# Optimization experiments

Measured on AMD Instinct MI355X. Metric: run time of the kernel, lower is better.

## Reference

```python
import jax, jax.numpy as jnp
import numpy as np

EMBED_DIM = 1024
NUM_HEADS = 16
HEAD_DIM = EMBED_DIM // NUM_HEADS


def setup_inputs() -> dict:
    key = jax.random.key(0)
    ks = jax.random.split(key, 9)
    s = 1.0 / np.sqrt(EMBED_DIM)
    x = jax.random.normal(ks[0], (2, 2048, EMBED_DIM), dtype=jnp.float32)
    Wq = jax.random.uniform(ks[1], (EMBED_DIM, EMBED_DIM), jnp.float32, -s, s)
    bq = jax.random.uniform(ks[2], (EMBED_DIM,), jnp.float32, -s, s)
    Wk = jax.random.uniform(ks[3], (EMBED_DIM, EMBED_DIM), jnp.float32, -s, s)
    bk = jax.random.uniform(ks[4], (EMBED_DIM,), jnp.float32, -s, s)
    Wv = jax.random.uniform(ks[5], (EMBED_DIM, EMBED_DIM), jnp.float32, -s, s)
    bv = jax.random.uniform(ks[6], (EMBED_DIM,), jnp.float32, -s, s)
    Wo = jax.random.uniform(ks[7], (EMBED_DIM, EMBED_DIM), jnp.float32, -s, s)
    bo = jax.random.uniform(ks[8], (EMBED_DIM,), jnp.float32, -s, s)
    return {"x": x, "Wq": Wq, "bq": bq, "Wk": Wk, "bk": bk,
            "Wv": Wv, "bv": bv, "Wo": Wo, "bo": bo}


def reference(x, Wq, bq, Wk, bk, Wv, bv, Wo, bo):
    B, N, C = x.shape
    H, D = NUM_HEADS, HEAD_DIM
    # nn.Linear: y = x @ W.T + b; here W stored as [in, out] so y = x @ W + b
    def split_heads(y):
        return y.reshape(B, N, H, D).transpose(0, 2, 1, 3)  # [B,H,N,D]
    q = split_heads(x @ Wq + bq)
    k = split_heads(x @ Wk + bk)
    v = split_heads(x @ Wv + bv)
    scores = jnp.einsum('bhnd,bhmd->bhnm', q, k) / jnp.sqrt(jnp.float32(D)).astype(x.dtype)
    attn = jax.nn.softmax(scores, axis=-1)
    ctx = jnp.einsum('bhnm,bhmd->bhnd', attn, v)
    ctx = ctx.transpose(0, 2, 1, 3).reshape(B, N, C)
    return ctx @ Wo + bo
```

## Files before the change

### kernel.cpp

```cpp
#include <hip/hip_runtime.h>
#include <hip/hip_bf16.h>
#include <stdint.h>
#include <stddef.h>

using bf16 = __hip_bfloat16;
using bf16x8 = __attribute__((ext_vector_type(8))) short;
using f32x4  = __attribute__((ext_vector_type(4))) float;
using f32x16 = __attribute__((ext_vector_type(16))) float;
typedef unsigned int u32x2 __attribute__((ext_vector_type(2)));
typedef unsigned int u32x4 __attribute__((ext_vector_type(4)));

#define MFMA16(a, b, c) __builtin_amdgcn_mfma_f32_16x16x32_bf16((a), (b), (c), 0, 0, 0)
#define MFMA32(a, b, c) __builtin_amdgcn_mfma_f32_32x32x16_bf16((a), (b), (c), 0, 0, 0)

#define GLD16(g, l)                                                            \
  __builtin_amdgcn_global_load_lds(                                            \
      (const __attribute__((address_space(1))) void*)(g),                      \
      (__attribute__((address_space(3))) void*)(l), 16, 0, 0)

__device__ __forceinline__ float exp2_fast(float x) {
#if __has_builtin(__builtin_amdgcn_exp2f)
  return __builtin_amdgcn_exp2f(x);
#else
  return __expf(x * 0.69314718056f);
#endif
}

__device__ __forceinline__ float fmax3(float a, float b, float c) {
  return fmaxf(fmaxf(a, b), c);
}

__device__ __forceinline__ unsigned int cvtpk_bf16(float lo, float hi) {
  unsigned int r;
  asm("v_cvt_pk_bf16_f32 %0, %1, %2" : "=v"(r) : "v"(lo), "v"(hi));
  return r;
}

__device__ __forceinline__ void permswap(unsigned int& a, unsigned int& b, int hi) {
#if __has_builtin(__builtin_amdgcn_permlane32_swap)
  u32x2 r = __builtin_amdgcn_permlane32_swap(a, b, false, false);
  a = r.x;
  b = r.y;
#else
  unsigned int sa = __shfl_xor((unsigned int)a, 32, 64);
  unsigned int sb = __shfl_xor((unsigned int)b, 32, 64);
  unsigned int an = hi ? sb : a;
  unsigned int bn = hi ? b : sa;
  a = an; b = bn;
#endif
}


__global__ void convert_x(const float* __restrict__ x, bf16* __restrict__ out) {
  const int i = blockIdx.x * 256 + threadIdx.x;
  const float4 v = ((const float4*)x)[i];
  __hip_bfloat162* o2 = (__hip_bfloat162*)(out + (size_t)i * 4);
  o2[0] = __float22bfloat162_rn(make_float2(v.x, v.y));
  o2[1] = __float22bfloat162_rn(make_float2(v.z, v.w));
}

__global__ void convert_w(const float* __restrict__ W0, const float* __restrict__ W1,
                          const float* __restrict__ W2, const float* __restrict__ W3,
                          bf16* __restrict__ Wt) {
  __shared__ float t[32][33];
  const int bx = blockIdx.x;
  const int mat = bx >> 10;
  const float* W = (mat == 0) ? W0 : (mat == 1) ? W1 : (mat == 2) ? W2 : W3;
  const int rem = bx & 1023;
  const int k0 = (rem >> 5) * 32, n0 = (rem & 31) * 32;
  const int c = threadIdx.x & 31, r0 = (threadIdx.x >> 5) * 4;
#pragma unroll
  for (int i = 0; i < 4; ++i) {
    const int r = r0 + i;
    t[r][c] = W[(size_t)(k0 + r) * 1024 + n0 + c];
  }
  __syncthreads();
  bf16* dst = Wt + (size_t)mat * 1024 * 1024;
#pragma unroll
  for (int i = 0; i < 4; ++i) {
    const int rn = r0 + i;
    dst[(size_t)(n0 + rn) * 1024 + k0 + c] = __float2bfloat16(t[c][rn]);
  }
}

__global__ void concat_bias(const float* __restrict__ bq, const float* __restrict__ bk,
                            const float* __restrict__ bv, const float* __restrict__ bo,
                            float* __restrict__ dst) {
  const int i = blockIdx.x * 256 + threadIdx.x;
  const float* src = (i < 1024) ? bq : (i < 2048) ? bk : (i < 3072) ? bv : bo;
  dst[i] = src[i & 1023];
}

__global__ __launch_bounds__(256)
void gemm_qkv(const bf16* __restrict__ A, const bf16* __restrict__ Bt,
              const float* __restrict__ bias,
              bf16* __restrict__ Qb, bf16* __restrict__ Kb, bf16* __restrict__ Vt,
              int K) {
  __shared__ bf16 As[3][128 * 32];
  __shared__ bf16 Bs[3][128 * 32];
  const int tid = threadIdx.x;
  const int lane = tid & 63, w = tid >> 6;
  const int wr = w >> 1, wc = w & 1;
  const int lrow = lane & 15, lgk = lane >> 4;
  const int bm = blockIdx.y * 128, bn = blockIdx.x * 128;
  f32x4 acc[4][4] = {};
  const bf16* Ab = A + (size_t)bm * K;
  const bf16* Bb = Bt + (size_t)bn * K;
  const int e0 = tid, e1 = 256 + tid;
  const int NT = K >> 5;

  auto stage = [&](int s, int k0) {
    GLD16(Ab + (size_t)(e0 >> 2) * K + k0 + (e0 & 3) * 8, &As[s][e0 * 8]);
    GLD16(Ab + (size_t)(e1 >> 2) * K + k0 + (e1 & 3) * 8, &As[s][e1 * 8]);
    GLD16(Bb + (size_t)(e0 >> 2) * K + k0 + (e0 & 3) * 8, &Bs[s][e0 * 8]);
    GLD16(Bb + (size_t)(e1 >> 2) * K + k0 + (e1 & 3) * 8, &Bs[s][e1 * 8]);
  };

  stage(0, 0);
  stage(1, 32);
  int cur = 0, nxt = 2;
  for (int t = 0; t < NT; ++t) {
    if (t < NT - 1)
      asm volatile("s_waitcnt vmcnt(4)" ::: "memory");
    else
      asm volatile("s_waitcnt vmcnt(0)" ::: "memory");
    __builtin_amdgcn_s_barrier();
    if (t + 2 < NT) {
      stage(nxt, (t + 2) << 5);
      nxt = (nxt == 2) ? 0 : nxt + 1;
    }
    bf16x8 af[4], bfr[4];
#pragma unroll
    for (int m = 0; m < 4; ++m)
      af[m] = *(const bf16x8*)(&As[cur][(wr * 64 + m * 16 + lrow) * 32 + lgk * 8]);
#pragma unroll
    for (int n = 0; n < 4; ++n)
      bfr[n] = *(const bf16x8*)(&Bs[cur][(wc * 64 + n * 16 + lrow) * 32 + lgk * 8]);
#pragma unroll
    for (int m = 0; m < 4; ++m)
#pragma unroll
      for (int n = 0; n < 4; ++n)
        acc[m][n] = MFMA16(af[m], bfr[n], acc[m][n]);
    cur = (cur == 2) ? 0 : cur + 1;
  }

#pragma unroll
  for (int m = 0; m < 4; ++m) {
#pragma unroll
    for (int n = 0; n < 4; ++n) {
      const int col = bn + wc * 64 + n * 16 + lrow;
      const float bv_ = bias[col];
      const int row0 = bm + wr * 64 + m * 16 + lgk * 4;
      const int which = col >> 10;
      const int hd = col & 1023;
      const int h = hd >> 6, d = hd & 63;
      const int b = row0 >> 11, t0 = row0 & 2047;
      const int bh = b * 16 + h;
      if (which == 2) {
        uint2 pk;
        pk.x = cvtpk_bf16(acc[m][n][0] + bv_, acc[m][n][1] + bv_);
        pk.y = cvtpk_bf16(acc[m][n][2] + bv_, acc[m][n][3] + bv_);
        *(uint2*)(Vt + ((size_t)bh * 64 + d) * 2048 + t0) = pk;
      } else if (which == 0) {
#pragma unroll
        for (int j = 0; j < 4; ++j)
          Qb[((size_t)bh * 2048 + t0 + j) * 64 + d] =
              __float2bfloat16((acc[m][n][j] + bv_) * 0.18033688f);
      } else {
#pragma unroll
        for (int j = 0; j < 4; ++j)
          Kb[((size_t)bh * 2048 + t0 + j) * 64 + d] =
              __float2bfloat16(acc[m][n][j] + bv_);
      }
    }
  }
}

__global__ __launch_bounds__(256)
void gemm_o(const bf16* __restrict__ A, const bf16* __restrict__ Bt,
            const float* __restrict__ bias, float* __restrict__ Of, int K) {
  __shared__ bf16 As[3][128 * 32];
  __shared__ bf16 Bs[3][64 * 32];
  const int tid = threadIdx.x;
  const int lane = tid & 63, w = tid >> 6;
  const int wr = w >> 1, wc = w & 1;
  const int lrow = lane & 15, lgk = lane >> 4;
  const int bm = blockIdx.y * 128, bn = blockIdx.x * 64;
  f32x4 acc[4][2] = {};
  const bf16* Ab = A + (size_t)bm * K;
  const bf16* Bb = Bt + (size_t)bn * K;
  const int e0 = tid, e1 = 256 + tid;
  const int NT = K >> 5;

  auto stage = [&](int s, int k0) {
    GLD16(Ab + (size_t)(e0 >> 2) * K + k0 + (e0 & 3) * 8, &As[s][e0 * 8]);
    GLD16(Ab + (size_t)(e1 >> 2) * K + k0 + (e1 & 3) * 8, &As[s][e1 * 8]);
    GLD16(Bb + (size_t)(e0 >> 2) * K + k0 + (e0 & 3) * 8, &Bs[s][e0 * 8]);
  };

  stage(0, 0);
  stage(1, 32);
  int cur = 0, nxt = 2;
  for (int t = 0; t < NT; ++t) {
    if (t < NT - 1)
      asm volatile("s_waitcnt vmcnt(3)" ::: "memory");
    else
      asm volatile("s_waitcnt vmcnt(0)" ::: "memory");
    __builtin_amdgcn_s_barrier();
    if (t + 2 < NT) {
      stage(nxt, (t + 2) << 5);
      nxt = (nxt == 2) ? 0 : nxt + 1;
    }
    bf16x8 af[4], bfr[2];
#pragma unroll
    for (int m = 0; m < 4; ++m)
      af[m] = *(const bf16x8*)(&As[cur][(wr * 64 + m * 16 + lrow) * 32 + lgk * 8]);
#pragma unroll
    for (int n = 0; n < 2; ++n)
      bfr[n] = *(const bf16x8*)(&Bs[cur][(wc * 32 + n * 16 + lrow) * 32 + lgk * 8]);
#pragma unroll
    for (int m = 0; m < 4; ++m)
#pragma unroll
      for (int n = 0; n < 2; ++n)
        acc[m][n] = MFMA16(af[m], bfr[n], acc[m][n]);
    cur = (cur == 2) ? 0 : cur + 1;
  }

#pragma unroll
  for (int m = 0; m < 4; ++m) {
#pragma unroll
    for (int n = 0; n < 2; ++n) {
      const int col = bn + wc * 32 + n * 16 + lrow;
      const float bv_ = bias[col];
      const int row0 = bm + wr * 64 + m * 16 + lgk * 4;
#pragma unroll
      for (int j = 0; j < 4; ++j)
        Of[(size_t)(row0 + j) * 1024 + col] = acc[m][n][j] + bv_;
    }
  }
}

__global__ __launch_bounds__(256, 2)
void attn_kernel(const bf16* __restrict__ Q, const bf16* __restrict__ Kb,
                 const bf16* __restrict__ Vt, bf16* __restrict__ ctx) {
  __shared__ bf16 Kl[3][64 * 64];
  __shared__ bf16 Vl[3][64 * 64];

  const int tid = threadIdx.x, lane = tid & 63, w = tid >> 6;
  const int lo5 = lane & 31, hi = lane >> 5;

  const int bid = blockIdx.x;
  const int xcd = bid & 7, idx = bid >> 3;
  const int bh = (xcd << 2) | (idx >> 4);
  const int qt = idx & 15;
  const int q0 = qt * 128 + w * 32;

  const bf16* Qbh = Q + (size_t)bh * 2048 * 64;
  const bf16* Kbh = Kb + (size_t)bh * 2048 * 64;
  const bf16* Vbh = Vt + (size_t)bh * 64 * 2048;

  bf16x8 qf[4];
#pragma unroll
  for (int f = 0; f < 4; ++f)
    qf[f] = *(const bf16x8*)(Qbh + (size_t)(q0 + lo5) * 64 + f * 16 + hi * 8);

  f32x16 o0 = {}, o1 = {};
  float m2 = -1e30f;
  float lsum = 0.f;

  auto stage = [&](int buf, int kv) {
#pragma unroll
    for (int i = 0; i < 2; ++i) {
      const int c = (w * 2 + i) * 64 + lane;
      const int r = c >> 3, j = c & 7;
      const int js = (j ^ (r & 7)) * 8;
      GLD16(Kbh + (size_t)(kv + r) * 64 + js, &Kl[buf][c * 8]);
      GLD16(Vbh + (size_t)r * 2048 + kv + js, &Vl[buf][c * 8]);
    }
  };

  bf16x8 pa[4];

  auto softmax_pa = [&](f32x16& s0, f32x16& s1) {
    float r1[11];
#pragma unroll
    for (int i = 0; i < 5; ++i)
      r1[i] = fmax3(s0[3 * i], s0[3 * i + 1], s0[3 * i + 2]);
    r1[5] = fmax3(s0[15], s1[0], s1[1]);
#pragma unroll
    for (int i = 0; i < 4; ++i)
      r1[6 + i] = fmax3(s1[2 + 3 * i], s1[3 + 3 * i], s1[4 + 3 * i]);
    r1[10] = fmaxf(s1[14], s1[15]);
    float r2[4];
#pragma unroll
    for (int i = 0; i < 3; ++i) r2[i] = fmax3(r1[3 * i], r1[3 * i + 1], r1[3 * i + 2]);
    r2[3] = fmaxf(r1[9], r1[10]);
    const float pm = fmaxf(fmax3(r2[0], r2[1], r2[2]), r2[3]);
    if (!__all(pm <= m2 + 11.5416f)) {
      const float mx = fmaxf(pm, __shfl_xor(pm, 32, 64));
      const float mn = fmaxf(m2, mx);
      const float corr = exp2_fast(m2 - mn);
      m2 = mn;
      lsum *= corr;
#pragma unroll
      for (int j = 0; j < 16; ++j) { o0[j] *= corr; o1[j] *= corr; }
    }
#pragma unroll
    for (int j = 0; j < 16; ++j) s0[j] = exp2_fast(s0[j] - m2);
#pragma unroll
    for (int j = 0; j < 16; ++j) s1[j] = exp2_fast(s1[j] - m2);
    float a8[8];
#pragma unroll
    for (int j = 0; j < 8; ++j) a8[j] = (s0[j] + s0[j + 8]) + (s1[j] + s1[j + 8]);
    float a4[4];
#pragma unroll
    for (int j = 0; j < 4; ++j) a4[j] = a8[j] + a8[j + 4];
    lsum += (a4[0] + a4[1]) + (a4[2] + a4[3]);
#pragma unroll
    for (int ks = 0; ks < 4; ++ks) {
      const f32x16& s = (ks < 2) ? s0 : s1;
      const int b0 = (ks & 1) * 8;
      unsigned int a0 = cvtpk_bf16(s[b0 + 0], s[b0 + 1]);
      unsigned int c0 = cvtpk_bf16(s[b0 + 4], s[b0 + 5]);
      unsigned int a1 = cvtpk_bf16(s[b0 + 2], s[b0 + 3]);
      unsigned int c1 = cvtpk_bf16(s[b0 + 6], s[b0 + 7]);
      permswap(a0, c0, hi);
      permswap(a1, c1, hi);
      u32x4 tt;
      tt.x = a0; tt.y = a1; tt.z = c0; tt.w = c1;
      pa[ks] = __builtin_bit_cast(bf16x8, tt);
    }
  };

  f32x16 sA0, sA1, sB0, sB1;
  bf16x8 vfA[8], vfB[8];
  int cur = 0, nxt = 2;

  auto step = [&](int t, f32x16& sC0, f32x16& sC1, bf16x8 (&vfC)[8],
                  f32x16& sP0, f32x16& sP1, bf16x8 (&vfP)[8]) {
    const int kv = t << 6;
    if (t < 31)
      asm volatile("s_waitcnt vmcnt(4)" ::: "memory");
    else
      asm volatile("s_waitcnt vmcnt(0)" ::: "memory");
    __builtin_amdgcn_s_barrier();
    if (t + 2 < 32) {
      stage(nxt, kv + 128);
      nxt = (nxt == 2) ? 0 : nxt + 1;
    }
    bf16x8 kf[8];
#pragma unroll
    for (int kt = 0; kt < 2; ++kt)
#pragma unroll
      for (int f = 0; f < 4; ++f) {
        const int r = kt * 32 + lo5;
        kf[kt * 4 + f] =
            *(const bf16x8*)(&Kl[cur][(r * 8 + (((f << 1) + hi) ^ (r & 7))) * 8]);
      }
#pragma unroll
    for (int dt = 0; dt < 2; ++dt)
#pragma unroll
      for (int ks = 0; ks < 4; ++ks) {
        const int r = dt * 32 + lo5;
        vfC[dt * 4 + ks] =
            *(const bf16x8*)(&Vl[cur][(r * 8 + (((ks << 1) + hi) ^ (r & 7))) * 8]);
      }
    if (t > 0) softmax_pa(sP0, sP1);
    __builtin_amdgcn_s_setprio(1);
    sC0 = f32x16{};
    sC1 = f32x16{};
#pragma unroll
    for (int f = 0; f < 4; ++f) sC0 = MFMA32(kf[f], qf[f], sC0);
#pragma unroll
    for (int f = 0; f < 4; ++f) sC1 = MFMA32(kf[4 + f], qf[f], sC1);
    if (t > 0) {
#pragma unroll
      for (int ks = 0; ks < 4; ++ks) {
        o0 = MFMA32(vfP[ks], pa[ks], o0);
        o1 = MFMA32(vfP[4 + ks], pa[ks], o1);
      }
    }
    __builtin_amdgcn_s_setprio(0);
    cur = (cur == 2) ? 0 : cur + 1;
  };

  stage(0, 0);
  stage(1, 64);

  step(0, sA0, sA1, vfA, sB0, sB1, vfB);
  for (int tt = 1; tt < 31; tt += 2) {
    step(tt, sB0, sB1, vfB, sA0, sA1, vfA);
    step(tt + 1, sA0, sA1, vfA, sB0, sB1, vfB);
  }
  step(31, sB0, sB1, vfB, sA0, sA1, vfA);

  softmax_pa(sB0, sB1);
#pragma unroll
  for (int ks = 0; ks < 4; ++ks) {
    o0 = MFMA32(vfB[ks], pa[ks], o0);
    o1 = MFMA32(vfB[4 + ks], pa[ks], o1);
  }

  lsum += __shfl_xor(lsum, 32, 64);
  const float inv = 1.f / lsum;
  const int b = bh >> 4, h = bh & 15;
  bf16* crow = ctx + (size_t)(b * 2048 + q0 + lo5) * 1024 + h * 64;
#pragma unroll
  for (int g = 0; g < 4; ++g) {
    uint2 pk0, pk1;
    pk0.x = cvtpk_bf16(o0[4 * g + 0] * inv, o0[4 * g + 1] * inv);
    pk0.y = cvtpk_bf16(o0[4 * g + 2] * inv, o0[4 * g + 3] * inv);
    pk1.x = cvtpk_bf16(o1[4 * g + 0] * inv, o1[4 * g + 1] * inv);
    pk1.y = cvtpk_bf16(o1[4 * g + 2] * inv, o1[4 * g + 3] * inv);
    *(uint2*)(crow + 8 * g + 4 * hi) = pk0;
    *(uint2*)(crow + 32 + 8 * g + 4 * hi) = pk1;
  }
}


extern "C" void kernel_launch(void* const* d_in, const int* in_sizes, int n_in,
                              void* d_out, int out_size, void* d_ws, size_t ws_size,
                              hipStream_t stream) {
  const float* x  = (const float*)d_in[0];
  const float* Wq = (const float*)d_in[1];
  const float* bq = (const float*)d_in[2];
  const float* Wk = (const float*)d_in[3];
  const float* bk = (const float*)d_in[4];
  const float* Wv = (const float*)d_in[5];
  const float* bv = (const float*)d_in[6];
  const float* Wo = (const float*)d_in[7];
  const float* bo = (const float*)d_in[8];
  float* out = (float*)d_out;

  char* ws = (char*)d_ws;
  bf16* xb  = (bf16*)(ws);
  bf16* Wt  = (bf16*)(ws + ((size_t)8 << 20));
  bf16* Qb  = (bf16*)(ws + ((size_t)16 << 20));
  bf16* Kb  = (bf16*)(ws + ((size_t)24 << 20));
  bf16* Vt  = (bf16*)(ws + ((size_t)32 << 20));
  bf16* ctx = (bf16*)(ws + ((size_t)40 << 20));
  float* ba = (float*)(ws + ((size_t)48 << 20));

  convert_x<<<dim3(4096), dim3(256), 0, stream>>>(x, xb);
  convert_w<<<dim3(4096), dim3(256), 0, stream>>>(Wq, Wk, Wv, Wo, Wt);
  concat_bias<<<dim3(16), dim3(256), 0, stream>>>(bq, bk, bv, bo, ba);

  gemm_qkv<<<dim3(24, 32), dim3(256), 0, stream>>>(xb, Wt, ba, Qb, Kb, Vt, 1024);

  attn_kernel<<<dim3(512), dim3(256), 0, stream>>>(Qb, Kb, Vt, ctx);

  gemm_o<<<dim3(16, 32), dim3(256), 0, stream>>>(
      ctx, Wt + (size_t)3072 * 1024, ba + 3072, out, 1024);
}
```

Measured before the change: 126.2 us.

## Enlarge QKV GEMM tiles to 256x256 with 8 waves and staged half-tile pipeline

```diff
diff --git a/kernel.cpp b/kernel.cpp
--- a/kernel.cpp
+++ b/kernel.cpp
@@ -91,86 +91,167 @@
   dst[i] = src[i & 1023];
 }
 
-__global__ __launch_bounds__(256)
+__global__ __launch_bounds__(512, 2)
 void gemm_qkv(const bf16* __restrict__ A, const bf16* __restrict__ Bt,
               const float* __restrict__ bias,
-              bf16* __restrict__ Qb, bf16* __restrict__ Kb, bf16* __restrict__ Vt,
-              int K) {
-  __shared__ bf16 As[3][128 * 32];
-  __shared__ bf16 Bs[3][128 * 32];
+              bf16* __restrict__ Qb, bf16* __restrict__ Kb, bf16* __restrict__ Vt) {
+  __shared__ bf16 Abuf[2][2][128 * 64];
+  __shared__ bf16 Bbuf[2][2][128 * 64];
   const int tid = threadIdx.x;
   const int lane = tid & 63, w = tid >> 6;
-  const int wr = w >> 1, wc = w & 1;
+  const int wr = w >> 2, wc = w & 3;
   const int lrow = lane & 15, lgk = lane >> 4;
-  const int bm = blockIdx.y * 128, bn = blockIdx.x * 128;
-  f32x4 acc[4][4] = {};
-  const bf16* Ab = A + (size_t)bm * K;
-  const bf16* Bb = Bt + (size_t)bn * K;
-  const int e0 = tid, e1 = 256 + tid;
-  const int NT = K >> 5;
-
-  auto stage = [&](int s, int k0) {
-    GLD16(Ab + (size_t)(e0 >> 2) * K + k0 + (e0 & 3) * 8, &As[s][e0 * 8]);
-    GLD16(Ab + (size_t)(e1 >> 2) * K + k0 + (e1 & 3) * 8, &As[s][e1 * 8]);
-    GLD16(Bb + (size_t)(e0 >> 2) * K + k0 + (e0 & 3) * 8, &Bs[s][e0 * 8]);
-    GLD16(Bb + (size_t)(e1 >> 2) * K + k0 + (e1 & 3) * 8, &Bs[s][e1 * 8]);
-  };
-
-  stage(0, 0);
-  stage(1, 32);
-  int cur = 0, nxt = 2;
-  for (int t = 0; t < NT; ++t) {
-    if (t < NT - 1)
-      asm volatile("s_waitcnt vmcnt(4)" ::: "memory");
-    else
+
+  const int bid = blockIdx.x;
+  const int xcd = bid & 7, i6 = bid >> 3;
+  const int xr = xcd >> 1, xc = xcd & 1;
+  const int bm = (xr * 4 + (i6 & 3)) * 256;
+  const int bn = (xc * 6 + (i6 >> 2)) * 256;
+
+  f32x4 acc[8][4] = {};
+
+  auto stageA = [&](int b, int hh, int kt) {
+#pragma unroll
+    for (int u = 0; u < 2; ++u) {
+      const int c = u * 512 + tid;
+      const int r = c >> 3, j = c & 7;
+      GLD16(A + (size_t)(bm + hh * 128 + r) * 1024 + kt * 64 + ((j ^ (r & 7)) * 8),
+            &Abuf[b][hh][c * 8]);
+    }
+  };
+  auto stageB = [&](int b, int hh, int kt) {
+#pragma unroll
+    for (int u = 0; u < 2; ++u) {
+      const int c = u * 512 + tid;
+      const int r = c >> 3, j = c & 7;
+      GLD16(Bt + (size_t)(bn + hh * 128 + r) * 1024 + kt * 64 + ((j ^ (r & 7)) * 8),
+            &Bbuf[b][hh][c * 8]);
+    }
+  };
+
+  bf16x8 a_[8];
+  bf16x8 b0_[4], b1_[4];
+
+  auto readA = [&](int b, int mg, bf16x8 (&dst)[8]) {
+#pragma unroll
+    for (int mf = 0; mf < 4; ++mf)
+#pragma unroll
+      for (int kk = 0; kk < 2; ++kk) {
+        const int r = (mg * 4 + mf) * 16 + lrow;
+        const int s = (kk * 4 + lgk) ^ (lrow & 7);
+        dst[mf * 2 + kk] = *(const bf16x8*)(&Abuf[b][wr][(r * 8 + s) * 8]);
+      }
+  };
+  auto readB = [&](int b, int ng, bf16x8 (&dst)[4]) {
+#pragma unroll
+    for (int nf = 0; nf < 2; ++nf)
+#pragma unroll
+      for (int kk = 0; kk < 2; ++kk) {
+        const int r = (wc & 1) * 64 + (ng * 2 + nf) * 16 + lrow;
+        const int s = (kk * 4 + lgk) ^ (lrow & 7);
+        dst[nf * 2 + kk] = *(const bf16x8*)(&Bbuf[b][wc >> 1][(r * 8 + s) * 8]);
+      }
+  };
+
+  stageA(0, 0, 0);
+  stageA(0, 1, 0);
+  stageB(0, 0, 0);
+  stageB(0, 1, 0);
+
+  for (int t = 0; t < 16; ++t) {
+    const int b = t & 1, nb = b ^ 1;
+    if (t < 15) {
+      stageA(nb, 0, t + 1);
+      asm volatile("s_waitcnt vmcnt(2)" ::: "memory");
+    } else {
       asm volatile("s_waitcnt vmcnt(0)" ::: "memory");
-    __builtin_amdgcn_s_barrier();
-    if (t + 2 < NT) {
-      stage(nxt, (t + 2) << 5);
-      nxt = (nxt == 2) ? 0 : nxt + 1;
-    }
-    bf16x8 af[4], bfr[4];
-#pragma unroll
-    for (int m = 0; m < 4; ++m)
-      af[m] = *(const bf16x8*)(&As[cur][(wr * 64 + m * 16 + lrow) * 32 + lgk * 8]);
-#pragma unroll
-    for (int n = 0; n < 4; ++n)
-      bfr[n] = *(const bf16x8*)(&Bs[cur][(wc * 64 + n * 16 + lrow) * 32 + lgk * 8]);
-#pragma unroll
-    for (int m = 0; m < 4; ++m)
-#pragma unroll
-      for (int n = 0; n < 4; ++n)
-        acc[m][n] = MFMA16(af[m], bfr[n], acc[m][n]);
-    cur = (cur == 2) ? 0 : cur + 1;
-  }
-
-#pragma unroll
-  for (int m = 0; m < 4; ++m) {
-#pragma unroll
-    for (int n = 0; n < 4; ++n) {
-      const int col = bn + wc * 64 + n * 16 + lrow;
+    }
+    __builtin_amdgcn_s_barrier();
+    readA(b, 0, a_);
+    readB(b, 0, b0_);
+    asm volatile("s_waitcnt lgkmcnt(0)" ::: "memory");
+    __builtin_amdgcn_sched_barrier(0);
+    __builtin_amdgcn_s_setprio(1);
+#pragma unroll
+    for (int mf = 0; mf < 4; ++mf)
+#pragma unroll
+      for (int nf = 0; nf < 2; ++nf)
+#pragma unroll
+        for (int kk = 0; kk < 2; ++kk)
+          acc[mf][nf] = MFMA16(a_[mf * 2 + kk], b0_[nf * 2 + kk], acc[mf][nf]);
+    __builtin_amdgcn_s_setprio(0);
+    __builtin_amdgcn_s_barrier();
+    readB(b, 1, b1_);
+    if (t < 15) stageA(nb, 1, t + 1);
+    __builtin_amdgcn_s_barrier();
+    asm volatile("s_waitcnt lgkmcnt(0)" ::: "memory");
+    __builtin_amdgcn_sched_barrier(0);
+    __builtin_amdgcn_s_setprio(1);
+#pragma unroll
+    for (int mf = 0; mf < 4; ++mf)
+#pragma unroll
+      for (int nf = 0; nf < 2; ++nf)
+#pragma unroll
+        for (int kk = 0; kk < 2; ++kk)
+          acc[mf][2 + nf] = MFMA16(a_[mf * 2 + kk], b1_[nf * 2 + kk], acc[mf][2 + nf]);
+    __builtin_amdgcn_s_setprio(0);
+    __builtin_amdgcn_s_barrier();
+    readA(b, 1, a_);
+    if (t < 15) stageB(nb, 0, t + 1);
+    __builtin_amdgcn_s_barrier();
+    asm volatile("s_waitcnt lgkmcnt(0)" ::: "memory");
+    __builtin_amdgcn_sched_barrier(0);
+    __builtin_amdgcn_s_setprio(1);
+#pragma unroll
+    for (int mf = 0; mf < 4; ++mf)
+#pragma unroll
+      for (int nf = 0; nf < 2; ++nf)
+#pragma unroll
+        for (int kk = 0; kk < 2; ++kk)
+          acc[4 + mf][2 + nf] =
+              MFMA16(a_[mf * 2 + kk], b1_[nf * 2 + kk], acc[4 + mf][2 + nf]);
+    __builtin_amdgcn_s_setprio(0);
+    __builtin_amdgcn_s_barrier();
+    if (t < 15) stageB(nb, 1, t + 1);
+    __builtin_amdgcn_s_setprio(1);
+#pragma unroll
+    for (int mf = 0; mf < 4; ++mf)
+#pragma unroll
+      for (int nf = 0; nf < 2; ++nf)
+#pragma unroll
+        for (int kk = 0; kk < 2; ++kk)
+          acc[4 + mf][nf] = MFMA16(a_[mf * 2 + kk], b0_[nf * 2 + kk], acc[4 + mf][nf]);
+    __builtin_amdgcn_s_setprio(0);
+    __builtin_amdgcn_s_barrier();
+  }
+
+  const int which = bn >> 10;
+#pragma unroll
+  for (int mf = 0; mf < 8; ++mf) {
+#pragma unroll
+    for (int nf = 0; nf < 4; ++nf) {
+      const int col = bn + wc * 64 + nf * 16 + lrow;
       const float bv_ = bias[col];
-      const int row0 = bm + wr * 64 + m * 16 + lgk * 4;
-      const int which = col >> 10;
+      const int row0 = bm + wr * 128 + mf * 16 + lgk * 4;
       const int hd = col & 1023;
       const int h = hd >> 6, d = hd & 63;
-      const int b = row0 >> 11, t0 = row0 & 2047;
-      const int bh = b * 16 + h;
+      const int bb = row0 >> 11, t0 = row0 & 2047;
+      const int bh = bb * 16 + h;
       if (which == 2) {
         uint2 pk;
-        pk.x = cvtpk_bf16(acc[m][n][0] + bv_, acc[m][n][1] + bv_);
-        pk.y = cvtpk_bf16(acc[m][n][2] + bv_, acc[m][n][3] + bv_);
+        pk.x = cvtpk_bf16(acc[mf][nf][0] + bv_, acc[mf][nf][1] + bv_);
+        pk.y = cvtpk_bf16(acc[mf][nf][2] + bv_, acc[mf][nf][3] + bv_);
         *(uint2*)(Vt + ((size_t)bh * 64 + d) * 2048 + t0) = pk;
       } else if (which == 0) {
 #pragma unroll
         for (int j = 0; j < 4; ++j)
           Qb[((size_t)bh * 2048 + t0 + j) * 64 + d] =
-              __float2bfloat16((acc[m][n][j] + bv_) * 0.18033688f);
+              __float2bfloat16((acc[mf][nf][j] + bv_) * 0.18033688f);
       } else {
 #pragma unroll
         for (int j = 0; j < 4; ++j)
           Kb[((size_t)bh * 2048 + t0 + j) * 64 + d] =
-              __float2bfloat16(acc[m][n][j] + bv_);
+              __float2bfloat16(acc[mf][nf][j] + bv_);
       }
     }
   }
@@ -243,8 +324,8 @@
 __global__ __launch_bounds__(256, 2)
 void attn_kernel(const bf16* __restrict__ Q, const bf16* __restrict__ Kb,
                  const bf16* __restrict__ Vt, bf16* __restrict__ ctx) {
-  __shared__ bf16 Kl[3][64 * 64];
-  __shared__ bf16 Vl[3][64 * 64];
+  __shared__ bf16 Kl[2][64 * 64];
+  __shared__ bf16 Vl[2][64 * 64];
 
   const int tid = threadIdx.x, lane = tid & 63, w = tid >> 6;
   const int lo5 = lane & 31, hi = lane >> 5;
@@ -334,20 +415,17 @@
 
   f32x16 sA0, sA1, sB0, sB1;
   bf16x8 vfA[8], vfB[8];
-  int cur = 0, nxt = 2;
 
   auto step = [&](int t, f32x16& sC0, f32x16& sC1, bf16x8 (&vfC)[8],
                   f32x16& sP0, f32x16& sP1, bf16x8 (&vfP)[8]) {
+    const int cur = t & 1;
     const int kv = t << 6;
+    if (t < 31) stage(cur ^ 1, kv + 64);
     if (t < 31)
       asm volatile("s_waitcnt vmcnt(4)" ::: "memory");
     else
       asm volatile("s_waitcnt vmcnt(0)" ::: "memory");
     __builtin_amdgcn_s_barrier();
-    if (t + 2 < 32) {
-      stage(nxt, kv + 128);
-      nxt = (nxt == 2) ? 0 : nxt + 1;
-    }
     bf16x8 kf[8];
 #pragma unroll
     for (int kt = 0; kt < 2; ++kt)
@@ -366,6 +444,9 @@
             *(const bf16x8*)(&Vl[cur][(r * 8 + (((ks << 1) + hi) ^ (r & 7))) * 8]);
       }
     if (t > 0) softmax_pa(sP0, sP1);
+    asm volatile("s_waitcnt lgkmcnt(0)" ::: "memory");
+    __builtin_amdgcn_sched_barrier(0);
+    __builtin_amdgcn_s_barrier();
     __builtin_amdgcn_s_setprio(1);
     sC0 = f32x16{};
     sC1 = f32x16{};
@@ -381,11 +462,9 @@
       }
     }
     __builtin_amdgcn_s_setprio(0);
-    cur = (cur == 2) ? 0 : cur + 1;
   };
 
   stage(0, 0);
-  stage(1, 64);
 
   step(0, sA0, sA1, vfA, sB0, sB1, vfB);
   for (int tt = 1; tt < 31; tt += 2) {
@@ -445,7 +524,7 @@
   convert_w<<<dim3(4096), dim3(256), 0, stream>>>(Wq, Wk, Wv, Wo, Wt);
   concat_bias<<<dim3(16), dim3(256), 0, stream>>>(bq, bk, bv, bo, ba);
 
-  gemm_qkv<<<dim3(24, 32), dim3(256), 0, stream>>>(xb, Wt, ba, Qb, Kb, Vt, 1024);
+  gemm_qkv<<<dim3(192), dim3(512), 0, stream>>>(xb, Wt, ba, Qb, Kb, Vt);
 
   attn_kernel<<<dim3(512), dim3(256), 0, stream>>>(Qb, Kb, Vt, ctx);
 
```

Measured after the change: 123.4 us. 2.2% less time.
